# Optimization experiments

Measured on AMD Instinct MI355X. Metric: run time of the kernel, lower is better.

Reference implementation:

```python
import jax, jax.numpy as jnp
import numpy as np

K = 3      # kernel size
P = 1      # padding
HEADS = 6  # num_heads


def setup_inputs() -> dict:
    key = jax.random.key(0)
    ks = jax.random.split(key, 6)
    B, H, W, C = 2, 48, 48, 192
    kk4h = K ** 4 * HEADS  # 486
    sc = 0.02
    return {
        "x": jax.random.normal(ks[0], (B, H, W, C), jnp.float32),
        "v_w": jax.random.normal(ks[1], (C, C), jnp.float32) * sc,
        "attn_w": jax.random.normal(ks[2], (kk4h, C), jnp.float32) * sc,
        "attn_b": jax.random.normal(ks[3], (kk4h,), jnp.float32) * sc,
        "proj_w": jax.random.normal(ks[4], (C, C), jnp.float32) * sc,
        "proj_b": jax.random.normal(ks[5], (C,), jnp.float32) * sc,
    }


def reference(x, v_w, attn_w, attn_b, proj_w, proj_b):
    # OutlookAttention with k=3, s=1 (pool is identity, h=H, w=W), p=1
    B, H, W, C = x.shape
    hd = C // HEADS
    scale = float(hd) ** -0.5

    # value projection (Linear, no bias): [B,H,W,C]
    v = x @ v_w.T

    # unfold: gather kxk neighborhood per pixel, row-major kernel order
    vp = jnp.pad(v, ((0, 0), (P, P), (P, P), (0, 0)))
    patches = jnp.stack(
        [vp[:, ki:ki + H, kj:kj + W, :] for ki in range(K) for kj in range(K)],
        axis=3,
    )  # [B,H,W,k*k,C]
    # -> [B, heads, hw, k*k, hd]
    v_ = patches.reshape(B, H * W, K * K, HEADS, hd).transpose(0, 3, 1, 2, 4)

    # attention logits from (pooled == identity) x: [B,H,W,k^4*heads]
    a = x @ attn_w.T + attn_b
    a = a.reshape(B, H * W, HEADS, K * K, K * K).transpose(0, 2, 1, 3, 4)
    a = jax.nn.softmax(a * scale, axis=-1)  # [B,heads,hw,kk,kk]

    # windowed attention
    out = jnp.einsum("bnlij,bnljd->bnlid", a, v_)  # [B,heads,hw,kk,hd]

    # fold (col2im): scatter-add each kernel tap back, then crop padding
    o = out.transpose(0, 2, 3, 1, 4).reshape(B, H, W, K * K, C)
    acc = jnp.zeros((B, H + 2 * P, W + 2 * P, C), dtype=o.dtype)
    idx = 0
    for ki in range(K):
        for kj in range(K):
            acc = acc.at[:, ki:ki + H, kj:kj + W, :].add(o[:, :, :, idx, :])
            idx += 1
    folded = acc[:, P:P + H, P:P + W, :]

    return folded @ proj_w.T + proj_b
```

## Files before the change

kernel.cpp:

```cpp
#include <hip/hip_runtime.h>

#define BB 2
#define HH 48
#define WW 48
#define CC 192
#define NHEADS 6
#define HD 32
#define KK 9
#define FF 486
#define NPIX (BB*HH*WW)
#define SCALE 0.17677669529663687f

typedef __bf16 bf16;
typedef __attribute__((ext_vector_type(4))) __bf16 bf16x4;
typedef __attribute__((ext_vector_type(8))) __bf16 bf16x8;
typedef __attribute__((ext_vector_type(4))) float f32x4;

#define KD 192
#define LDA 200

__global__ __launch_bounds__(256) void gemm_va_kernel(
    const float* __restrict__ x, const float* __restrict__ vw,
    const float* __restrict__ aw, const float* __restrict__ ab,
    float* __restrict__ v, float* __restrict__ a)
{
    __shared__ bf16 As[64][LDA];
    __shared__ bf16 Bs[64][LDA];
    const int t = threadIdx.x;
    const int m0 = blockIdx.x * 64;
    const int by = blockIdx.y;
    const bool is_v = (by < 3);
    const int n0 = is_v ? by * 64 : (by - 3) * 64;
    const int Ndim = is_v ? CC : FF;
    const float* W = is_v ? vw : aw;
    float* OUT = is_v ? v : a;

    #pragma unroll
    for (int i = 0; i < 12; ++i) {
        const int f = t + i * 256;
        const int row = f / 48, c4 = f % 48;
        const float4 xv = *(const float4*)(x + (size_t)(m0 + row) * KD + c4 * 4);
        bf16x4 tv = { (__bf16)xv.x, (__bf16)xv.y, (__bf16)xv.z, (__bf16)xv.w };
        *(bf16x4*)(&As[row][c4 * 4]) = tv;
    }
    #pragma unroll
    for (int i = 0; i < 12; ++i) {
        const int f = t + i * 256;
        const int row = f / 48, c4 = f % 48;
        float4 wv = make_float4(0.f, 0.f, 0.f, 0.f);
        if (n0 + row < Ndim)
            wv = *(const float4*)(W + (size_t)(n0 + row) * KD + c4 * 4);
        bf16x4 tv = { (__bf16)wv.x, (__bf16)wv.y, (__bf16)wv.z, (__bf16)wv.w };
        *(bf16x4*)(&Bs[row][c4 * 4]) = tv;
    }
    __syncthreads();

    const int wave = t >> 6, lane = t & 63;
    const int wm = (wave >> 1) * 32;
    const int wn = (wave & 1) * 32;
    const int lrow = lane & 15;
    const int lk   = (lane >> 4) * 8;

    f32x4 acc[2][2] = {};
    #pragma unroll
    for (int ks = 0; ks < 6; ++ks) {
        bf16x8 afr[2], bfr[2];
        #pragma unroll
        for (int j = 0; j < 2; ++j) {
            afr[j] = *(const bf16x8*)(&As[wm + j * 16 + lrow][ks * 32 + lk]);
            bfr[j] = *(const bf16x8*)(&Bs[wn + j * 16 + lrow][ks * 32 + lk]);
        }
        #pragma unroll
        for (int i = 0; i < 2; ++i)
            #pragma unroll
            for (int j = 0; j < 2; ++j)
                acc[i][j] = __builtin_amdgcn_mfma_f32_16x16x32_bf16(afr[i], bfr[j], acc[i][j], 0, 0, 0);
    }

    const int crow = (lane >> 4) * 4;
    #pragma unroll
    for (int j = 0; j < 2; ++j) {
        const int col = n0 + wn + j * 16 + lrow;
        if (col < Ndim) {
            const float bv = is_v ? 0.f : ab[col];
            #pragma unroll
            for (int i = 0; i < 2; ++i) {
                #pragma unroll
                for (int r = 0; r < 4; ++r) {
                    const int row = m0 + wm + i * 16 + crow + r;
                    OUT[(size_t)row * Ndim + col] = acc[i][j][r] + bv;
                }
            }
        }
    }
}

__global__ void attn_kernel(const float* __restrict__ v, const float* __restrict__ a,
                            float* __restrict__ o) {
    int n = blockIdx.x;
    int tid = threadIdx.x;
    int b = n / (HH * WW), rem = n % (HH * WW), h = rem / WW, w = rem % WW;
    __shared__ float p[FF];
    __shared__ float vl[KK][CC];

    for (int f = tid; f < FF; f += CC) p[f] = a[n * FF + f];
    #pragma unroll
    for (int j = 0; j < KK; ++j) {
        int hh = h + j / 3 - 1, ww = w + j % 3 - 1;
        if (hh >= 0 && hh < HH && ww >= 0 && ww < WW)
            vl[j][tid] = v[((b * HH + hh) * WW + ww) * CC + tid];
        else
            vl[j][tid] = 0.f;
    }
    __syncthreads();

    if (tid < NHEADS * KK) {
        float* row = p + tid * KK;
        float t[KK];
        float m = -1e30f;
        #pragma unroll
        for (int j = 0; j < KK; ++j) { t[j] = row[j] * SCALE; m = fmaxf(m, t[j]); }
        float s = 0.f;
        #pragma unroll
        for (int j = 0; j < KK; ++j) { t[j] = __expf(t[j] - m); s += t[j]; }
        float inv = 1.f / s;
        #pragma unroll
        for (int j = 0; j < KK; ++j) row[j] = t[j] * inv;
    }
    __syncthreads();

    int head = tid / HD;
    const float* ph = p + head * 81;
    #pragma unroll
    for (int i = 0; i < KK; ++i) {
        float acc = 0.f;
        #pragma unroll
        for (int j = 0; j < KK; ++j) acc += ph[i * 9 + j] * vl[j][tid];
        o[(n * KK + i) * CC + tid] = acc;
    }
}

__global__ __launch_bounds__(256) void proj_fold_kernel(
    const float* __restrict__ o, const float* __restrict__ pw,
    const float* __restrict__ pb, float* __restrict__ out)
{
    __shared__ bf16 As[32][LDA];
    __shared__ bf16 Bs[64][LDA];
    const int t = threadIdx.x;
    const int m0 = blockIdx.x * 32;
    const int n0 = blockIdx.y * 64;

    for (int i = 0; i < 6; ++i) {
        const int f = t + i * 256;
        const int row = f / 48, c4 = f % 48;
        const int n = m0 + row;
        const int b = n / (HH * WW), r2 = n % (HH * WW), y = r2 / WW, x = r2 % WW;
        float4 s = make_float4(0.f, 0.f, 0.f, 0.f);
        for (int ki = 0; ki < 3; ++ki) {
            const int gy = y + 1 - ki;
            if (gy < 0 || gy >= HH) continue;
            for (int kj = 0; kj < 3; ++kj) {
                const int gx = x + 1 - kj;
                if (gx < 0 || gx >= WW) continue;
                const float4 ov = *(const float4*)(
                    o + (((size_t)(b * HH + gy) * WW + gx) * KK + ki * 3 + kj) * CC + c4 * 4);
                s.x += ov.x; s.y += ov.y; s.z += ov.z; s.w += ov.w;
            }
        }
        bf16x4 tv = { (__bf16)s.x, (__bf16)s.y, (__bf16)s.z, (__bf16)s.w };
        *(bf16x4*)(&As[row][c4 * 4]) = tv;
    }
    #pragma unroll
    for (int i = 0; i < 12; ++i) {
        const int f = t + i * 256;
        const int row = f / 48, c4 = f % 48;
        const float4 wv = *(const float4*)(pw + (size_t)(n0 + row) * KD + c4 * 4);
        bf16x4 tv = { (__bf16)wv.x, (__bf16)wv.y, (__bf16)wv.z, (__bf16)wv.w };
        *(bf16x4*)(&Bs[row][c4 * 4]) = tv;
    }
    __syncthreads();

    const int wave = t >> 6, lane = t & 63;
    const int wm = (wave & 1) * 16;
    const int wn = (wave >> 1) * 32;
    const int lrow = lane & 15;
    const int lk   = (lane >> 4) * 8;

    f32x4 acc[2] = {};
    #pragma unroll
    for (int ks = 0; ks < 6; ++ks) {
        bf16x8 afr = *(const bf16x8*)(&As[wm + lrow][ks * 32 + lk]);
        #pragma unroll
        for (int j = 0; j < 2; ++j) {
            bf16x8 bfr = *(const bf16x8*)(&Bs[wn + j * 16 + lrow][ks * 32 + lk]);
            acc[j] = __builtin_amdgcn_mfma_f32_16x16x32_bf16(afr, bfr, acc[j], 0, 0, 0);
        }
    }

    const int crow = (lane >> 4) * 4;
    #pragma unroll
    for (int j = 0; j < 2; ++j) {
        const int col = n0 + wn + j * 16 + lrow;
        const float bv = pb[col];
        #pragma unroll
        for (int r = 0; r < 4; ++r) {
            const int row = m0 + wm + crow + r;
            out[(size_t)row * CC + col] = acc[j][r] + bv;
        }
    }
}

extern "C" void kernel_launch(void* const* d_in, const int* in_sizes, int n_in,
                              void* d_out, int out_size, void* d_ws, size_t ws_size,
                              hipStream_t stream) {
    const float* x   = (const float*)d_in[0];
    const float* vw  = (const float*)d_in[1];
    const float* aw  = (const float*)d_in[2];
    const float* ab  = (const float*)d_in[3];
    const float* pw  = (const float*)d_in[4];
    const float* pb  = (const float*)d_in[5];
    float* out = (float*)d_out;

    float* v = (float*)d_ws;
    float* a = v + (size_t)NPIX * CC;
    float* o = a + (size_t)NPIX * FF;

    dim3 blk(256);
    dim3 grid_va(NPIX / 64, 3 + 8);
    dim3 grid_pj(NPIX / 32, CC / 64);

    gemm_va_kernel<<<grid_va, blk, 0, stream>>>(x, vw, aw, ab, v, a);
    attn_kernel<<<NPIX, CC, 0, stream>>>(v, a, o);
    proj_fold_kernel<<<grid_pj, blk, 0, stream>>>(o, pw, pb, out);
}
```

Baseline: 116.5 us.

## Store v and per-tap outputs in bf16 and split fold into its own kernel

Result: faster. 104.5 us (-10.4%).

```diff
diff --git a/kernel.cpp b/kernel.cpp
--- a/kernel.cpp
+++ b/kernel.cpp
@@ -12,6 +12,7 @@
 #define SCALE 0.17677669529663687f
 
 typedef __bf16 bf16;
+typedef __attribute__((ext_vector_type(2))) __bf16 bf16x2;
 typedef __attribute__((ext_vector_type(4))) __bf16 bf16x4;
 typedef __attribute__((ext_vector_type(8))) __bf16 bf16x8;
 typedef __attribute__((ext_vector_type(4))) float f32x4;
@@ -22,7 +23,7 @@
 __global__ __launch_bounds__(256) void gemm_va_kernel(
     const float* __restrict__ x, const float* __restrict__ vw,
     const float* __restrict__ aw, const float* __restrict__ ab,
-    float* __restrict__ v, float* __restrict__ a)
+    bf16* __restrict__ v, float* __restrict__ a)
 {
     __shared__ bf16 As[64][LDA];
     __shared__ bf16 Bs[64][LDA];
@@ -33,7 +34,6 @@
     const int n0 = is_v ? by * 64 : (by - 3) * 64;
     const int Ndim = is_v ? CC : FF;
     const float* W = is_v ? vw : aw;
-    float* OUT = is_v ? v : a;
 
     #pragma unroll
     for (int i = 0; i < 12; ++i) {
@@ -78,25 +78,38 @@
     }
 
     const int crow = (lane >> 4) * 4;
-    #pragma unroll
-    for (int j = 0; j < 2; ++j) {
-        const int col = n0 + wn + j * 16 + lrow;
-        if (col < Ndim) {
-            const float bv = is_v ? 0.f : ab[col];
+    if (is_v) {
+        #pragma unroll
+        for (int j = 0; j < 2; ++j) {
+            const int col = n0 + wn + j * 16 + lrow;
             #pragma unroll
-            for (int i = 0; i < 2; ++i) {
+            for (int i = 0; i < 2; ++i)
                 #pragma unroll
                 for (int r = 0; r < 4; ++r) {
                     const int row = m0 + wm + i * 16 + crow + r;
-                    OUT[(size_t)row * Ndim + col] = acc[i][j][r] + bv;
+                    v[(size_t)row * CC + col] = (__bf16)acc[i][j][r];
                 }
+        }
+    } else {
+        #pragma unroll
+        for (int j = 0; j < 2; ++j) {
+            const int col = n0 + wn + j * 16 + lrow;
+            if (col < FF) {
+                const float bv = ab[col];
+                #pragma unroll
+                for (int i = 0; i < 2; ++i)
+                    #pragma unroll
+                    for (int r = 0; r < 4; ++r) {
+                        const int row = m0 + wm + i * 16 + crow + r;
+                        a[(size_t)row * FF + col] = acc[i][j][r] + bv;
+                    }
             }
         }
     }
 }
 
-__global__ void attn_kernel(const float* __restrict__ v, const float* __restrict__ a,
-                            float* __restrict__ o) {
+__global__ void attn_kernel(const bf16* __restrict__ v, const float* __restrict__ a,
+                            bf16* __restrict__ o) {
     int n = blockIdx.x;
     int tid = threadIdx.x;
     int b = n / (HH * WW), rem = n % (HH * WW), h = rem / WW, w = rem % WW;
@@ -108,7 +121,7 @@
     for (int j = 0; j < KK; ++j) {
         int hh = h + j / 3 - 1, ww = w + j % 3 - 1;
         if (hh >= 0 && hh < HH && ww >= 0 && ww < WW)
-            vl[j][tid] = v[((b * HH + hh) * WW + ww) * CC + tid];
+            vl[j][tid] = (float)v[((size_t)(b * HH + hh) * WW + ww) * CC + tid];
         else
             vl[j][tid] = 0.f;
     }
@@ -136,12 +149,34 @@
         float acc = 0.f;
         #pragma unroll
         for (int j = 0; j < KK; ++j) acc += ph[i * 9 + j] * vl[j][tid];
-        o[(n * KK + i) * CC + tid] = acc;
-    }
-}
-
-__global__ __launch_bounds__(256) void proj_fold_kernel(
-    const float* __restrict__ o, const float* __restrict__ pw,
+        o[((size_t)n * KK + i) * CC + tid] = (__bf16)acc;
+    }
+}
+
+__global__ void fold_kernel(const bf16x2* __restrict__ o, bf16x2* __restrict__ folded) {
+    const int idx = blockIdx.x * blockDim.x + threadIdx.x;
+    const int c2 = idx % 96, n = idx / 96;
+    const int b = n / (HH * WW), rem = n % (HH * WW), y = rem / WW, x = rem % WW;
+    float s0 = 0.f, s1 = 0.f;
+    #pragma unroll
+    for (int ki = 0; ki < 3; ++ki) {
+        const int gy = y + 1 - ki;
+        if (gy < 0 || gy >= HH) continue;
+        #pragma unroll
+        for (int kj = 0; kj < 3; ++kj) {
+            const int gx = x + 1 - kj;
+            if (gx < 0 || gx >= WW) continue;
+            const size_t ps = (size_t)(b * HH + gy) * WW + gx;
+            const bf16x2 ov = o[(ps * KK + ki * 3 + kj) * 96 + c2];
+            s0 += (float)ov.x; s1 += (float)ov.y;
+        }
+    }
+    bf16x2 r = { (__bf16)s0, (__bf16)s1 };
+    folded[(size_t)n * 96 + c2] = r;
+}
+
+__global__ __launch_bounds__(256) void proj_kernel(
+    const bf16* __restrict__ folded, const float* __restrict__ pw,
     const float* __restrict__ pb, float* __restrict__ out)
 {
     __shared__ bf16 As[32][LDA];
@@ -150,25 +185,12 @@
     const int m0 = blockIdx.x * 32;
     const int n0 = blockIdx.y * 64;
 
-    for (int i = 0; i < 6; ++i) {
-        const int f = t + i * 256;
-        const int row = f / 48, c4 = f % 48;
-        const int n = m0 + row;
-        const int b = n / (HH * WW), r2 = n % (HH * WW), y = r2 / WW, x = r2 % WW;
-        float4 s = make_float4(0.f, 0.f, 0.f, 0.f);
-        for (int ki = 0; ki < 3; ++ki) {
-            const int gy = y + 1 - ki;
-            if (gy < 0 || gy >= HH) continue;
-            for (int kj = 0; kj < 3; ++kj) {
-                const int gx = x + 1 - kj;
-                if (gx < 0 || gx >= WW) continue;
-                const float4 ov = *(const float4*)(
-                    o + (((size_t)(b * HH + gy) * WW + gx) * KK + ki * 3 + kj) * CC + c4 * 4);
-                s.x += ov.x; s.y += ov.y; s.z += ov.z; s.w += ov.w;
-            }
-        }
-        bf16x4 tv = { (__bf16)s.x, (__bf16)s.y, (__bf16)s.z, (__bf16)s.w };
-        *(bf16x4*)(&As[row][c4 * 4]) = tv;
+    #pragma unroll
+    for (int i = 0; i < 3; ++i) {
+        const int f = t + i * 256;
+        const int row = f / 24, c8 = f % 24;
+        const bf16x8 av = *(const bf16x8*)(folded + (size_t)(m0 + row) * KD + c8 * 8);
+        *(bf16x8*)(&As[row][c8 * 8]) = av;
     }
     #pragma unroll
     for (int i = 0; i < 12; ++i) {
@@ -221,9 +243,10 @@
     const float* pb  = (const float*)d_in[5];
     float* out = (float*)d_out;
 
-    float* v = (float*)d_ws;
-    float* a = v + (size_t)NPIX * CC;
-    float* o = a + (size_t)NPIX * FF;
+    float* a      = (float*)d_ws;
+    bf16* v       = (bf16*)(a + (size_t)NPIX * FF);
+    bf16* o       = v + (size_t)NPIX * CC;
+    bf16* folded  = o + (size_t)NPIX * KK * CC;
 
     dim3 blk(256);
     dim3 grid_va(NPIX / 64, 3 + 8);
@@ -231,5 +254,6 @@
 
     gemm_va_kernel<<<grid_va, blk, 0, stream>>>(x, vw, aw, ab, v, a);
     attn_kernel<<<NPIX, CC, 0, stream>>>(v, a, o);
-    proj_fold_kernel<<<grid_pj, blk, 0, stream>>>(o, pw, pb, out);
-}
+    fold_kernel<<<(NPIX * 96) / 256, blk, 0, stream>>>((const bf16x2*)o, (bf16x2*)folded);
+    proj_kernel<<<grid_pj, blk, 0, stream>>>(folded, pw, pb, out);
+}
```
